# Performance work log

Hardware: AMD Instinct MI355X
Metric: run time of the kernel (lower is better)

Reference implementation:

```python
import jax, jax.numpy as jnp
import numpy as np
from jax import lax

HID = 128      # GNN hidden dim (node_label_embedding_size)
EMB = 64       # char-CNN output (graph_node_label_representation_size)
N_LAYERS = 6
N_ETYPES = 12
CHAR_EMB = 16
KW = 5         # conv kernel width
LEAKY = 0.2


def _gru(x, h, k, rk, b):
    # keras-style GRU cell: gates z, r, candidate hh; new h = z*h + (1-z)*hh
    H = h.shape[-1]
    g = x @ k + b                       # [N, 3H]
    z = jax.nn.sigmoid(g[:, :H] + h @ rk[:, :H])
    r = jax.nn.sigmoid(g[:, H:2 * H] + h @ rk[:, H:2 * H])
    hh = jnp.tanh(g[:, 2 * H:] + (r * h) @ rk[:, 2 * H:])
    return z * h + (1.0 - z) * hh


def setup_inputs() -> dict:
    key = jax.random.key(0)
    ks = jax.random.split(key, 32)
    N, U, L, E, G = 100000, 20000, 16, 100000, 64
    inp = {}
    inp["graphs_in_batch"] = G
    inp["node_labels_unique"] = jax.random.randint(ks[0], (U, L), 0, 256, dtype=jnp.int32)
    inp["node_labels_index"] = jax.random.randint(ks[1], (N,), 0, U, dtype=jnp.int32)
    inp["node_to_graph"] = jnp.sort(jax.random.randint(ks[2], (N,), 0, G, dtype=jnp.int32))
    inp["regression_labels"] = jax.random.normal(ks[3], (G,), dtype=jnp.float32)
    for t in range(N_ETYPES):
        inp[f"adj_{t}"] = jax.random.randint(ks[4 + t], (E, 2), 0, N, dtype=jnp.int32)
    # learned params
    inp["char_embed"] = jax.random.normal(ks[16], (256, CHAR_EMB), dtype=jnp.float32) * 0.1
    inp["conv_w"] = jax.random.normal(ks[17], (KW, CHAR_EMB, EMB), dtype=jnp.float32) / np.sqrt(KW * CHAR_EMB)
    inp["conv_b"] = jnp.zeros((EMB,), dtype=jnp.float32)
    inp["W_msg"] = jax.random.normal(ks[18], (N_LAYERS, N_ETYPES, HID, HID), dtype=jnp.float32) / np.sqrt(HID)
    inp["gru_k"] = jax.random.normal(ks[19], (N_LAYERS, HID, 3 * HID), dtype=jnp.float32) / np.sqrt(HID)
    inp["gru_rk"] = jax.random.normal(ks[20], (N_LAYERS, HID, 3 * HID), dtype=jnp.float32) / np.sqrt(HID)
    inp["gru_b"] = jnp.zeros((N_LAYERS, 3 * HID), dtype=jnp.float32)
    inp["score_w"] = jax.random.normal(ks[21], (HID, 1), dtype=jnp.float32) / np.sqrt(HID)
    inp["score_b"] = jnp.zeros((1,), dtype=jnp.float32)
    inp["mlp_w1"] = jax.random.normal(ks[22], (HID, 128), dtype=jnp.float32) / np.sqrt(HID)
    inp["mlp_b1"] = jnp.zeros((128,), dtype=jnp.float32)
    inp["mlp_w2"] = jax.random.normal(ks[23], (128, 32), dtype=jnp.float32) / np.sqrt(128)
    inp["mlp_b2"] = jnp.zeros((32,), dtype=jnp.float32)
    inp["mlp_w3"] = jax.random.normal(ks[24], (32, 8), dtype=jnp.float32) / np.sqrt(32)
    inp["mlp_b3"] = jnp.zeros((8,), dtype=jnp.float32)
    inp["mlp_w4"] = jax.random.normal(ks[25], (8, 1), dtype=jnp.float32) / np.sqrt(8)
    inp["mlp_b4"] = jnp.zeros((1,), dtype=jnp.float32)
    return inp


def reference(graphs_in_batch, node_labels_unique, node_labels_index, node_to_graph,
              regression_labels, adj_0, adj_1, adj_2, adj_3, adj_4, adj_5, adj_6,
              adj_7, adj_8, adj_9, adj_10, adj_11, char_embed, conv_w, conv_b,
              W_msg, gru_k, gru_rk, gru_b, score_w, score_b,
              mlp_w1, mlp_b1, mlp_w2, mlp_b2, mlp_w3, mlp_b3, mlp_w4, mlp_b4):
    adj = jnp.stack([adj_0, adj_1, adj_2, adj_3, adj_4, adj_5, adj_6,
                     adj_7, adj_8, adj_9, adj_10, adj_11])  # [T, E, 2]
    # --- char-CNN node label embedding ---
    chars = char_embed[node_labels_unique]                  # [U, L, CE]
    conv = lax.conv_general_dilated(chars, conv_w, (1,), 'SAME',
                                    dimension_numbers=('NWC', 'WIO', 'NWC'))
    label_rep = jnp.max(jax.nn.relu(conv + conv_b), axis=1)  # [U, EMB]
    feats = label_rep[node_labels_index]                     # [N, EMB]
    N = feats.shape[0]
    # pad initial features up to hidden_dim
    h = jnp.pad(feats, ((0, 0), (0, HID - EMB)))             # [N, HID]
    src = adj[:, :, 0]                                       # [T, E]
    tgt = adj[:, :, 1].reshape(-1)                           # [T*E]
    # --- 6-layer GGNN message passing ---
    for layer in range(N_LAYERS):
        h_src = h[src]                                       # [T, E, HID]
        msgs = jnp.einsum('teh,thd->ted', h_src, W_msg[layer])
        agg = jax.ops.segment_sum(msgs.reshape(-1, HID), tgt, num_segments=N)
        h = _gru(agg, h, gru_k[layer], gru_rk[layer], gru_b[layer])
    # --- weighted-sum graph readout (sigmoid weights, leaky_relu MLP) ---
    scores = jax.nn.sigmoid(h @ score_w + score_b)           # [N, 1]
    v = jax.nn.leaky_relu(h @ mlp_w1 + mlp_b1, LEAKY)
    v = jax.nn.leaky_relu(v @ mlp_w2 + mlp_b2, LEAKY)
    v = jax.nn.leaky_relu(v @ mlp_w3 + mlp_b3, LEAKY)
    v = v @ mlp_w4 + mlp_b4                                  # [N, 1]
    graph_rep = jax.ops.segment_sum(scores * v, node_to_graph,
                                    num_segments=graphs_in_batch)  # [G, 1]
    return graph_rep
```

## Files before the change

kernel.cpp:

```cpp
#include <hip/hip_runtime.h>
#include <hip/hip_bf16.h>

#define LEAKY_SLOPE 0.2f

typedef short short8 __attribute__((ext_vector_type(8)));
typedef float f32x4 __attribute__((ext_vector_type(4)));

static inline int cdiv(int a, int b) { return (a + b - 1) / b; }

__device__ __forceinline__ float bf2f(unsigned short s) {
    return __uint_as_float(((unsigned int)s) << 16);
}
__device__ __forceinline__ unsigned short f2bf(float x) {
    unsigned int u = __float_as_uint(x);
    return (unsigned short)((u + 0x7FFFu + ((u >> 16) & 1u)) >> 16);
}
__device__ __forceinline__ unsigned short bf_hi(float x, float& rem) {
    unsigned int u = __float_as_uint(x);
    unsigned int hi = (u + 0x7FFFu + ((u >> 16) & 1u)) & 0xFFFF0000u;
    rem = x - __uint_as_float(hi);
    return (unsigned short)(hi >> 16);
}

struct EdgeArgs {
    const int* adj[12];
    int E[12];
    int colOff[12];
};
struct ColPtrs { const int* c[12]; };
struct MutColPtrs { int* c[12]; };

__global__ __launch_bounds__(64) void label_kernel(
    const int* __restrict__ labels, const float* __restrict__ char_embed,
    const float* __restrict__ conv_w, const float* __restrict__ conv_b,
    float* __restrict__ lr, int U)
{
    __shared__ float ch[20][16];
    __shared__ int lab[16];
    const int u = blockIdx.x, t = threadIdx.x;
    {
        const int r = t >> 4, i = t & 15;
        const int padrow[4] = {0, 1, 18, 19};
        ch[padrow[r]][i] = 0.f;
    }
    if (t < 16) lab[t] = labels[(size_t)u * 16 + t];
    float cwr[5][16];
    #pragma unroll
    for (int k = 0; k < 5; ++k)
        #pragma unroll
        for (int i = 0; i < 16; ++i)
            cwr[k][i] = conv_w[(k * 16 + i) * 64 + t];
    __syncthreads();
    for (int j = t; j < 256; j += 64)
        ch[2 + (j >> 4)][j & 15] = char_embed[(size_t)lab[j >> 4] * 16 + (j & 15)];
    __syncthreads();
    float aw[16];
    const float b = conv_b[t];
    #pragma unroll
    for (int w = 0; w < 16; ++w) aw[w] = b;
    #pragma unroll
    for (int x = 0; x < 20; ++x)
        #pragma unroll
        for (int i = 0; i < 16; ++i) {
            const float chv = ch[x][i];
            #pragma unroll
            for (int k = 0; k < 5; ++k) {
                const int w = x - k;
                if (w >= 0 && w < 16) aw[w] += chv * cwr[k][i];
            }
        }
    float m = 0.f;
    #pragma unroll
    for (int w = 0; w < 16; ++w) m = fmaxf(m, aw[w]);
    lr[(size_t)u * 64 + t] = m;
}

__global__ void init_hP(const int* __restrict__ idx, const float* __restrict__ lr,
                        unsigned short* __restrict__ hP, int N, int NP)
{
    const int i = blockIdx.x * blockDim.x + threadIdx.x;
    if (i >= NP * 16) return;
    const int n = i >> 4, kg = i & 15;
    short8 hi, lo;
    #pragma unroll
    for (int j = 0; j < 8; ++j) { hi[j] = 0; lo[j] = 0; }
    if (n < N && kg < 8) {
        const int id = idx[n];
        #pragma unroll
        for (int j = 0; j < 8; ++j) {
            const float v = lr[(size_t)id * 64 + kg * 8 + j];
            float r; hi[j] = (short)bf_hi(v, r); lo[j] = (short)f2bf(r);
        }
    }
    *(short8*)(hP + (size_t)n * 256 + kg * 16) = hi;
    *(short8*)(hP + (size_t)n * 256 + kg * 16 + 8) = lo;
}

__global__ void hist_kernel(EdgeArgs ea, int* __restrict__ deg, int N)
{
    const int t = blockIdx.y;
    const int e = blockIdx.x * blockDim.x + threadIdx.x;
    if (e >= ea.E[t]) return;
    atomicAdd(&deg[(size_t)t * N + ea.adj[t][2 * e + 1]], 1);
}

__global__ __launch_bounds__(256) void scan_a(const int* __restrict__ deg,
                                              int* __restrict__ partial, int N, int nchunk)
{
    const int t = blockIdx.y, b = blockIdx.x;
    const int base = b * 2048;
    int s = 0;
    for (int i = threadIdx.x; i < 2048; i += 256) {
        const int g = base + i;
        if (g < N) s += deg[(size_t)t * N + g];
    }
    __shared__ int sm[256];
    sm[threadIdx.x] = s; __syncthreads();
    for (int off = 128; off > 0; off >>= 1) {
        if (threadIdx.x < off) sm[threadIdx.x] += sm[threadIdx.x + off];
        __syncthreads();
    }
    if (threadIdx.x == 0) partial[t * nchunk + b] = sm[0];
}

__global__ void scan_b(int* __restrict__ partial, int nchunk)
{
    const int t = threadIdx.x;
    if (t >= 12) return;
    int off = 0;
    for (int i = 0; i < nchunk; ++i) {
        const int s = partial[t * nchunk + i];
        partial[t * nchunk + i] = off;
        off += s;
    }
}

__global__ __launch_bounds__(256) void scan_c(const int* __restrict__ deg,
                                              const int* __restrict__ partial,
                                              int* __restrict__ rowptr, int N, int nchunk)
{
    const int t = blockIdx.y, b = blockIdx.x;
    int* rp = rowptr + (size_t)t * (N + 1);
    const int base = b * 2048;
    int v[8]; int s = 0;
    #pragma unroll
    for (int j = 0; j < 8; ++j) {
        const int g = base + threadIdx.x * 8 + j;
        v[j] = (g < N) ? deg[(size_t)t * N + g] : 0;
        s += v[j];
    }
    __shared__ int ts[256];
    ts[threadIdx.x] = s; __syncthreads();
    for (int off = 1; off < 256; off <<= 1) {
        const int val = (threadIdx.x >= off) ? ts[threadIdx.x - off] : 0;
        __syncthreads();
        ts[threadIdx.x] += val;
        __syncthreads();
    }
    int run = partial[t * nchunk + b] + (threadIdx.x ? ts[threadIdx.x - 1] : 0);
    #pragma unroll
    for (int j = 0; j < 8; ++j) {
        const int g = base + threadIdx.x * 8 + j;
        run += v[j];
        if (g < N) rp[g + 1] = run;
    }
    if (b == 0 && threadIdx.x == 0) rp[0] = 0;
}

__global__ void fill_kernel(EdgeArgs ea, const int* __restrict__ rowptr,
                            int* __restrict__ cursor, int* __restrict__ col, int N)
{
    const int t = blockIdx.y;
    const int e = blockIdx.x * blockDim.x + threadIdx.x;
    if (e >= ea.E[t]) return;
    const int s  = ea.adj[t][2 * e];
    const int tg = ea.adj[t][2 * e + 1];
    const int pos = rowptr[(size_t)t * (N + 1) + tg] + atomicAdd(&cursor[(size_t)t * N + tg], 1);
    col[ea.colOff[t] + pos] = s;
}

__global__ __launch_bounds__(256) void sort_cols_kernel(
    const int* __restrict__ rowptr, MutColPtrs mc, int N)
{
    const int t = blockIdx.y;
    const int r = blockIdx.x * blockDim.x + threadIdx.x;
    if (r >= N) return;
    int* c = mc.c[t];
    const int s = rowptr[(size_t)t * (N + 1) + r];
    const int e = rowptr[(size_t)t * (N + 1) + r + 1];
    for (int i = s + 1; i < e; ++i) {
        const int key = c[i];
        int j = i - 1;
        while (j >= s && c[j] > key) { c[j + 1] = c[j]; --j; }
        c[j + 1] = key;
    }
}

struct WSrc { const float* wmsg; const float* gk; const float* grk; const float* w1; };

__global__ void split_w_kernel(WSrc s, unsigned short* __restrict__ wb, int nmat)
{
    const int gidx = blockIdx.x * 256 + threadIdx.x;
    const int m = gidx >> 14, e = gidx & 16383;
    if (m >= nmat) return;
    const int kg = e >> 10, rem = e & 1023, c = rem >> 3, j = rem & 7;
    const int k = kg * 8 + j;
    float x;
    if (m < 72) x = s.wmsg[(size_t)m * 16384 + (size_t)k * 128 + c];
    else if (m < 108) {
        const int g = m - 72, layer = g / 6, r2 = g % 6;
        const float* base = (r2 < 3) ? s.gk : s.grk;
        const int slice = r2 % 3;
        x = base[(size_t)layer * 49152 + (size_t)k * 384 + slice * 128 + c];
    } else x = s.w1[(size_t)k * 128 + c];
    float r; const unsigned short hi = bf_hi(x, r);
    wb[(size_t)m * 32768 + e] = hi;
    wb[(size_t)m * 32768 + 16384 + e] = f2bf(r);
}

__global__ __launch_bounds__(256) void agg_kernel(
    const unsigned short* __restrict__ hP,
    const int* __restrict__ rowptr, ColPtrs cps,
    const unsigned short* __restrict__ wbL,
    float* __restrict__ agg, int N)
{
    __shared__ unsigned short Sf[32768];
    const int tid = threadIdx.x, p = blockIdx.x;
    const int R0 = p * 128;
    const int wave = tid >> 6, lane = tid & 63;
    const int wr = wave >> 1, wc = wave & 1, lrow = lane & 15, lkg = lane >> 4;
    const int rhalf = tid >> 2;
    const int j4 = tid & 3;
    f32x4 acc[4][4] = {};

    for (int t = 0; t < 12; ++t) {
        const int* __restrict__ rp_t = rowptr + (size_t)t * (N + 1);
        const int* __restrict__ cl = cps.c[t];
        #pragma unroll
        for (int half = 0; half < 2; ++half) {
            const int row = half * 64 + rhalf;
            const int R = R0 + row;
            float ga[32];
            #pragma unroll
            for (int j = 0; j < 32; ++j) ga[j] = 0.f;
            if (R < N) {
                const int e1 = rp_t[R + 1];
                for (int e = rp_t[R]; e < e1; ++e) {
                    const unsigned short* hp = hP + (size_t)cl[e] * 256 + j4 * 64;
                    #pragma unroll
                    for (int c = 0; c < 4; ++c) {
                        const short8 hh = *(const short8*)(hp + c * 16);
                        const short8 hl = *(const short8*)(hp + c * 16 + 8);
                        #pragma unroll
                        for (int q = 0; q < 8; ++q)
                            ga[c * 8 + q] += bf2f((unsigned short)hh[q])
                                           + bf2f((unsigned short)hl[q]);
                    }
                }
            }
            #pragma unroll
            for (int c = 0; c < 4; ++c) {
                const int kg = j4 * 4 + c;
                short8 hi, lo;
                #pragma unroll
                for (int q = 0; q < 8; ++q) {
                    float rem;
                    hi[q] = (short)bf_hi(ga[c * 8 + q], rem);
                    lo[q] = (short)f2bf(rem);
                }
                const int u = ((kg << 10) + row * 8) ^ (kg << 3);
                *(short8*)(Sf + u) = hi;
                *(short8*)(Sf + u + 16384) = lo;
            }
        }
        __syncthreads();
        {
            const unsigned short* __restrict__ B = wbL + (size_t)t * 32768;
            #pragma unroll
            for (int q = 0; q < 4; ++q) {
                const int kg = q * 4 + lkg;
                short8 ah[4], al[4];
                #pragma unroll
                for (int m = 0; m < 4; ++m) {
                    const int u = ((kg << 10) + (wr * 64 + m * 16 + lrow) * 8) ^ (kg << 3);
                    ah[m] = *(const short8*)(Sf + u);
                    al[m] = *(const short8*)(Sf + u + 16384);
                }
                #pragma unroll
                for (int n = 0; n < 4; ++n) {
                    const int ub = kg * 1024 + (wc * 64 + n * 16 + lrow) * 8;
                    const short8 bh = *(const short8*)(B + ub);
                    const short8 bl = *(const short8*)(B + ub + 16384);
                    #pragma unroll
                    for (int m = 0; m < 4; ++m) {
                        acc[m][n] = __builtin_amdgcn_mfma_f32_16x16x32_bf16(ah[m], bh, acc[m][n], 0, 0, 0);
                        acc[m][n] = __builtin_amdgcn_mfma_f32_16x16x32_bf16(ah[m], bl, acc[m][n], 0, 0, 0);
                        acc[m][n] = __builtin_amdgcn_mfma_f32_16x16x32_bf16(al[m], bh, acc[m][n], 0, 0, 0);
                    }
                }
            }
        }
        __syncthreads();
    }

    #pragma unroll
    for (int m = 0; m < 4; ++m)
        #pragma unroll
        for (int n = 0; n < 4; ++n) {
            const int col = wc * 64 + n * 16 + lrow;
            #pragma unroll
            for (int i = 0; i < 4; ++i) {
                const size_t Rg = (size_t)p * 128 + wr * 64 + m * 16 + lkg * 4 + i;
                agg[Rg * 128 + col] = acc[m][n][i];
            }
        }
}

__global__ __launch_bounds__(256) void zr2_kernel(
    const float* __restrict__ aggf, const unsigned short* __restrict__ hP,
    const unsigned short* __restrict__ k0, const unsigned short* __restrict__ k1,
    const unsigned short* __restrict__ rk0, const unsigned short* __restrict__ rk1,
    const float* __restrict__ bias,
    float* __restrict__ Zf, unsigned short* __restrict__ rhP)
{
    __shared__ unsigned short lds[2][8192];
    const int tid = threadIdx.x, p = blockIdx.x;
    const int wave = tid >> 6, lane = tid & 63;
    const int wr = wave >> 1, wc = wave & 1, lrow = lane & 15, lkg = lane >> 4;
    f32x4 acc[2][4][4] = {};
    float fv[16];
    short8 ph[2], pl[2];

    auto ldq = [&](int s) {
        const int q = s & 3;
        #pragma unroll
        for (int j = 0; j < 2; ++j) {
            const int cid = j * 256 + tid, kgl = cid >> 7, row = cid & 127;
            if (s < 4) {
                const float* a = aggf + ((size_t)p * 128 + row) * 128 + q * 32 + kgl * 8;
                const float4 v0 = *(const float4*)(a);
                const float4 v1 = *(const float4*)(a + 4);
                fv[j*8+0]=v0.x; fv[j*8+1]=v0.y; fv[j*8+2]=v0.z; fv[j*8+3]=v0.w;
                fv[j*8+4]=v1.x; fv[j*8+5]=v1.y; fv[j*8+6]=v1.z; fv[j*8+7]=v1.w;
            } else {
                const unsigned short* hp = hP + ((size_t)p * 128 + row) * 256 + (q * 4 + kgl) * 16;
                ph[j] = *(const short8*)(hp);
                pl[j] = *(const short8*)(hp + 8);
            }
        }
    };
    auto stq = [&](int buf, int s) {
        unsigned short* L = lds[buf];
        #pragma unroll
        for (int j = 0; j < 2; ++j) {
            const int cid = j * 256 + tid, kgl = cid >> 7, row = cid & 127;
            const int u = (kgl * 1024 + row * 8) ^ (kgl << 3);
            short8 hi, lo;
            if (s < 4) {
                #pragma unroll
                for (int q8 = 0; q8 < 8; ++q8) {
                    float rem; hi[q8] = (short)bf_hi(fv[j*8+q8], rem); lo[q8] = (short)f2bf(rem);
                }
            } else { hi = ph[j]; lo = pl[j]; }
            *(short8*)(L + u) = hi;
            *(short8*)(L + u + 4096) = lo;
        }
    };
    auto mfma_q = [&](int buf, int s) {
        const unsigned short* L = lds[buf];
        const int q = s & 3;
        short8 ah[4], al[4];
        #pragma unroll
        for (int m = 0; m < 4; ++m) {
            const int u = ((lkg << 10) + (wr * 64 + m * 16 + lrow) * 8) ^ (lkg << 3);
            ah[m] = *(const short8*)(L + u);
            al[m] = *(const short8*)(L + u + 4096);
        }
        const unsigned short* Bt[2] = { (s < 4) ? k0 : rk0, (s < 4) ? k1 : rk1 };
        #pragma unroll
        for (int t = 0; t < 2; ++t) {
            const unsigned short* __restrict__ B = Bt[t];
            #pragma unroll
            for (int n = 0; n < 4; ++n) {
                const int ub = (q * 4 + lkg) * 1024 + (wc * 64 + n * 16 + lrow) * 8;
                const short8 bh = *(const short8*)(B + ub);
                const short8 bl = *(const short8*)(B + ub + 16384);
                #pragma unroll
                for (int m = 0; m < 4; ++m) {
                    acc[t][m][n] = __builtin_amdgcn_mfma_f32_16x16x32_bf16(ah[m], bh, acc[t][m][n], 0, 0, 0);
                    acc[t][m][n] = __builtin_amdgcn_mfma_f32_16x16x32_bf16(ah[m], bl, acc[t][m][n], 0, 0, 0);
                    acc[t][m][n] = __builtin_amdgcn_mfma_f32_16x16x32_bf16(al[m], bh, acc[t][m][n], 0, 0, 0);
                }
            }
        }
    };

    ldq(0); stq(0, 0); ldq(1);
    __syncthreads();
    #pragma unroll
    for (int s = 0; s < 8; ++s) {
        mfma_q(s & 1, s);
        if (s < 7) {
            stq((s + 1) & 1, s + 1);
            if (s < 6) ldq(s + 2);
            __syncthreads();
        }
    }

    #pragma unroll
    for (int m = 0; m < 4; ++m)
        #pragma unroll
        for (int n = 0; n < 4; ++n) {
            const int col = wc * 64 + n * 16 + lrow;
            #pragma unroll
            for (int i = 0; i < 4; ++i) {
                const int rl = wr * 64 + m * 16 + lkg * 4 + i;
                const size_t R = (size_t)p * 128 + rl;
                const float z = 1.f / (1.f + __expf(-(acc[0][m][n][i] + bias[col])));
                Zf[R * 128 + col] = z;
                const float r = 1.f / (1.f + __expf(-(acc[1][m][n][i] + bias[128 + col])));
                const size_t hu = R * 256 + (size_t)(col >> 3) * 16 + (col & 7);
                const float h = bf2f(hP[hu]) + bf2f(hP[hu + 8]);
                float rem; const unsigned short hh = bf_hi(r * h, rem);
                rhP[hu] = hh;
                rhP[hu + 8] = f2bf(rem);
            }
        }
}

__global__ __launch_bounds__(256) void g2_kernel(
    const float* __restrict__ aggf, const unsigned short* __restrict__ rhP,
    const unsigned short* __restrict__ k2, const unsigned short* __restrict__ rk2,
    const float* __restrict__ bias, const float* __restrict__ Zf,
    unsigned short* __restrict__ hP)
{
    __shared__ unsigned short lds[2][8192];
    const int tid = threadIdx.x, p = blockIdx.x;
    const int wave = tid >> 6, lane = tid & 63;
    const int wr = wave >> 1, wc = wave & 1, lrow = lane & 15, lkg = lane >> 4;
    f32x4 acc[4][4] = {};
    float fv[16];
    short8 ph[2], pl[2];

    auto ldq = [&](int s) {
        const int q = s & 3;
        #pragma unroll
        for (int j = 0; j < 2; ++j) {
            const int cid = j * 256 + tid, kgl = cid >> 7, row = cid & 127;
            if (s < 4) {
                const float* a = aggf + ((size_t)p * 128 + row) * 128 + q * 32 + kgl * 8;
                const float4 v0 = *(const float4*)(a);
                const float4 v1 = *(const float4*)(a + 4);
                fv[j*8+0]=v0.x; fv[j*8+1]=v0.y; fv[j*8+2]=v0.z; fv[j*8+3]=v0.w;
                fv[j*8+4]=v1.x; fv[j*8+5]=v1.y; fv[j*8+6]=v1.z; fv[j*8+7]=v1.w;
            } else {
                const unsigned short* hp = rhP + ((size_t)p * 128 + row) * 256 + (q * 4 + kgl) * 16;
                ph[j] = *(const short8*)(hp);
                pl[j] = *(const short8*)(hp + 8);
            }
        }
    };
    auto stq = [&](int buf, int s) {
        unsigned short* L = lds[buf];
        #pragma unroll
        for (int j = 0; j < 2; ++j) {
            const int cid = j * 256 + tid, kgl = cid >> 7, row = cid & 127;
            const int u = (kgl * 1024 + row * 8) ^ (kgl << 3);
            short8 hi, lo;
            if (s < 4) {
                #pragma unroll
                for (int q8 = 0; q8 < 8; ++q8) {
                    float rem; hi[q8] = (short)bf_hi(fv[j*8+q8], rem); lo[q8] = (short)f2bf(rem);
                }
            } else { hi = ph[j]; lo = pl[j]; }
            *(short8*)(L + u) = hi;
            *(short8*)(L + u + 4096) = lo;
        }
    };
    auto mfma_q = [&](int buf, int s) {
        const unsigned short* L = lds[buf];
        const int q = s & 3;
        short8 ah[4], al[4];
        #pragma unroll
        for (int m = 0; m < 4; ++m) {
            const int u = ((lkg << 10) + (wr * 64 + m * 16 + lrow) * 8) ^ (lkg << 3);
            ah[m] = *(const short8*)(L + u);
            al[m] = *(const short8*)(L + u + 4096);
        }
        const unsigned short* __restrict__ B = (s < 4) ? k2 : rk2;
        #pragma unroll
        for (int n = 0; n < 4; ++n) {
            const int ub = (q * 4 + lkg) * 1024 + (wc * 64 + n * 16 + lrow) * 8;
            const short8 bh = *(const short8*)(B + ub);
            const short8 bl = *(const short8*)(B + ub + 16384);
            #pragma unroll
            for (int m = 0; m < 4; ++m) {
                acc[m][n] = __builtin_amdgcn_mfma_f32_16x16x32_bf16(ah[m], bh, acc[m][n], 0, 0, 0);
                acc[m][n] = __builtin_amdgcn_mfma_f32_16x16x32_bf16(ah[m], bl, acc[m][n], 0, 0, 0);
                acc[m][n] = __builtin_amdgcn_mfma_f32_16x16x32_bf16(al[m], bh, acc[m][n], 0, 0, 0);
            }
        }
    };

    ldq(0); stq(0, 0); ldq(1);
    __syncthreads();
    #pragma unroll
    for (int s = 0; s < 8; ++s) {
        mfma_q(s & 1, s);
        if (s < 7) {
            stq((s + 1) & 1, s + 1);
            if (s < 6) ldq(s + 2);
            __syncthreads();
        }
    }

    #pragma unroll
    for (int m = 0; m < 4; ++m)
        #pragma unroll
        for (int n = 0; n < 4; ++n) {
            const int col = wc * 64 + n * 16 + lrow;
            #pragma unroll
            for (int i = 0; i < 4; ++i) {
                const int rl = wr * 64 + m * 16 + lkg * 4 + i;
                const size_t R = (size_t)p * 128 + rl;
                const float g = acc[m][n][i] + bias[col];
                const size_t hu = R * 256 + (size_t)(col >> 3) * 16 + (col & 7);
                const float h = bf2f(hP[hu]) + bf2f(hP[hu + 8]);
                const float z = Zf[R * 128 + col];
                const float hn = z * h + (1.f - z) * tanhf(g);
                float rem; const unsigned short hh = bf_hi(hn, rem);
                hP[hu] = hh;
                hP[hu + 8] = f2bf(rem);
            }
        }
}

__global__ __launch_bounds__(256) void v1_kernel(
    const unsigned short* __restrict__ hP, const unsigned short* __restrict__ w1b,
    const float* __restrict__ bias, float* __restrict__ outF)
{
    __shared__ unsigned short lds[2][8192];
    const int tid = threadIdx.x, p = blockIdx.x;
    const int wave = tid >> 6, lane = tid & 63;
    const int wr = wave >> 1, wc = wave & 1, lrow = lane & 15, lkg = lane >> 4;
    f32x4 acc[4][4] = {};
    short8 ph[2], pl[2];

    auto ldq = [&](int s) {
        #pragma unroll
        for (int j = 0; j < 2; ++j) {
            const int cid = j * 256 + tid, kgl = cid >> 7, row = cid & 127;
            const unsigned short* hp = hP + ((size_t)p * 128 + row) * 256 + (s * 4 + kgl) * 16;
            ph[j] = *(const short8*)(hp);
            pl[j] = *(const short8*)(hp + 8);
        }
    };
    auto stq = [&](int buf) {
        unsigned short* L = lds[buf];
        #pragma unroll
        for (int j = 0; j < 2; ++j) {
            const int cid = j * 256 + tid, kgl = cid >> 7, row = cid & 127;
            const int u = (kgl * 1024 + row * 8) ^ (kgl << 3);
            *(short8*)(L + u) = ph[j];
            *(short8*)(L + u + 4096) = pl[j];
        }
    };
    auto mfma_q = [&](int buf, int s) {
        const unsigned short* L = lds[buf];
        short8 ah[4], al[4];
        #pragma unroll
        for (int m = 0; m < 4; ++m) {
            const int u = ((lkg << 10) + (wr * 64 + m * 16 + lrow) * 8) ^ (lkg << 3);
            ah[m] = *(const short8*)(L + u);
            al[m] = *(const short8*)(L + u + 4096);
        }
        #pragma unroll
        for (int n = 0; n < 4; ++n) {
            const int ub = (s * 4 + lkg) * 1024 + (wc * 64 + n * 16 + lrow) * 8;
            const short8 bh = *(const short8*)(w1b + ub);
            const short8 bl = *(const short8*)(w1b + ub + 16384);
            #pragma unroll
            for (int m = 0; m < 4; ++m) {
                acc[m][n] = __builtin_amdgcn_mfma_f32_16x16x32_bf16(ah[m], bh, acc[m][n], 0, 0, 0);
                acc[m][n] = __builtin_amdgcn_mfma_f32_16x16x32_bf16(ah[m], bl, acc[m][n], 0, 0, 0);
                acc[m][n] = __builtin_amdgcn_mfma_f32_16x16x32_bf16(al[m], bh, acc[m][n], 0, 0, 0);
            }
        }
    };

    ldq(0); stq(0); ldq(1);
    __syncthreads();
    #pragma unroll
    for (int s = 0; s < 4; ++s) {
        mfma_q(s & 1, s);
        if (s < 3) {
            stq((s + 1) & 1);
            if (s < 2) ldq(s + 2);
            __syncthreads();
        }
    }

    #pragma unroll
    for (int m = 0; m < 4; ++m)
        #pragma unroll
        for (int n = 0; n < 4; ++n) {
            const int col = wc * 64 + n * 16 + lrow;
            #pragma unroll
            for (int i = 0; i < 4; ++i) {
                const size_t R = (size_t)p * 128 + wr * 64 + m * 16 + lkg * 4 + i;
                float v = acc[m][n][i] + bias[col];
                v = v > 0.f ? v : LEAKY_SLOPE * v;
                outF[R * 128 + col] = v;
            }
        }
}

__global__ __launch_bounds__(256) void final_kernel(
    const unsigned short* __restrict__ hP, const float* __restrict__ V1,
    const int* __restrict__ n2g,
    const float* __restrict__ w2, const float* __restrict__ b2,
    const float* __restrict__ w3, const float* __restrict__ b3,
    const float* __restrict__ w4, const float* __restrict__ b4,
    const float* __restrict__ score_w, const float* __restrict__ score_b,
    float* __restrict__ out, int N)
{
    const int n = blockIdx.x * blockDim.x + threadIdx.x;
    const int nc = n < N ? n : N - 1;
    const int g = n2g[nc];

    float sp = score_b[0];
    #pragma unroll 4
    for (int kg = 0; kg < 16; ++kg) {
        const size_t hu = (size_t)nc * 256 + kg * 16;
        const short8 hh = *(const short8*)(hP + hu);
        const short8 hl = *(const short8*)(hP + hu + 8);
        #pragma unroll
        for (int j = 0; j < 8; ++j)
            sp += (bf2f((unsigned short)hh[j]) + bf2f((unsigned short)hl[j])) * score_w[kg * 8 + j];
    }

    float V2[32];
    #pragma unroll
    for (int j = 0; j < 32; ++j) V2[j] = b2[j];
    #pragma unroll 2
    for (int k = 0; k < 128; k += 4) {
        const float4 v1 = *reinterpret_cast<const float4*>(V1 + (size_t)nc * 128 + k);
        const float vv[4] = {v1.x, v1.y, v1.z, v1.w};
        #pragma unroll
        for (int kk = 0; kk < 4; ++kk)
            #pragma unroll
            for (int j = 0; j < 32; ++j)
                V2[j] += vv[kk] * w2[(k + kk) * 32 + j];
    }
    #pragma unroll
    for (int j = 0; j < 32; ++j) { const float x = V2[j]; V2[j] = x > 0.f ? x : LEAKY_SLOPE * x; }

    float V3[8];
    #pragma unroll
    for (int j = 0; j < 8; ++j) V3[j] = b3[j];
    #pragma unroll
    for (int k = 0; k < 32; ++k)
        #pragma unroll
        for (int j = 0; j < 8; ++j) V3[j] += V2[k] * w3[k * 8 + j];
    #pragma unroll
    for (int j = 0; j < 8; ++j) { const float x = V3[j]; V3[j] = x > 0.f ? x : LEAKY_SLOPE * x; }

    float o4 = b4[0];
    #pragma unroll
    for (int j = 0; j < 8; ++j) o4 += V3[j] * w4[j];

    const float sc = 1.f / (1.f + __expf(-sp));
    float val = (n < N) ? sc * o4 : 0.f;

    const int g0 = __shfl(g, 0, 64);
    if (__all(g == g0)) {
        #pragma unroll
        for (int d = 32; d > 0; d >>= 1) val += __shfl_xor(val, d, 64);
        if ((threadIdx.x & 63) == 0) unsafeAtomicAdd(out + g0, val);
    } else {
        if (n < N) unsafeAtomicAdd(out + g, val);
    }
}

extern "C" void kernel_launch(void* const* d_in, const int* in_sizes, int n_in,
                              void* d_out, int out_size, void* d_ws, size_t ws_size,
                              hipStream_t stream)
{
    (void)n_in;
    const int* labels   = (const int*)d_in[1];
    const int* nidx     = (const int*)d_in[2];
    const int* n2g      = (const int*)d_in[3];
    EdgeArgs ea;
    int Emax = 0, Etot = 0;
    for (int t = 0; t < 12; ++t) {
        ea.adj[t] = (const int*)d_in[5 + t];
        ea.E[t] = in_sizes[5 + t] / 2;
        ea.colOff[t] = Etot;
        Etot += ea.E[t];
        if (ea.E[t] > Emax) Emax = ea.E[t];
    }
    const float* char_embed = (const float*)d_in[17];
    const float* conv_w     = (const float*)d_in[18];
    const float* conv_b     = (const float*)d_in[19];
    const float* W_msg      = (const float*)d_in[20];
    const float* gru_k      = (const float*)d_in[21];
    const float* gru_rk     = (const float*)d_in[22];
    const float* gru_b      = (const float*)d_in[23];
    const float* score_w    = (const float*)d_in[24];
    const float* score_b    = (const float*)d_in[25];
    const float* w1 = (const float*)d_in[26];
    const float* b1 = (const float*)d_in[27];
    const float* w2 = (const float*)d_in[28];
    const float* b2 = (const float*)d_in[29];
    const float* w3 = (const float*)d_in[30];
    const float* b3 = (const float*)d_in[31];
    const float* w4 = (const float*)d_in[32];
    const float* b4 = (const float*)d_in[33];

    const int N = in_sizes[2];
    const int U = in_sizes[1] / 16;
    const int G = out_size;
    float* out = (float*)d_out;

    const int NPB = cdiv(N, 128);
    const int NP  = NPB * 128;
    const int NCHUNK = cdiv(N, 2048);
    const int NMAT = 109;

    float* ws = (float*)d_ws;
    size_t o = 0;
    float* lr   = ws + o; o += (size_t)U * 64;
    float* hPf  = ws + o; o += (size_t)NP * 128;
    float* aggf = ws + o; o += (size_t)NP * 128;
    float* Zf   = ws + o; o += (size_t)NP * 128;
    float* rhPf = ws + o; o += (size_t)NP * 128;
    float* wbf  = ws + o; o += (size_t)NMAT * 16384;
    int* rowptr = (int*)(ws + o);
    int* colarr = rowptr + (size_t)12 * (N + 1);
    const size_t total_bytes = o * sizeof(float)
        + ((size_t)12 * (N + 1) + (size_t)Etot) * sizeof(int);
    if (total_bytes > ws_size) return;

    unsigned short* hP  = (unsigned short*)hPf;
    unsigned short* rhP = (unsigned short*)rhPf;
    unsigned short* wb  = (unsigned short*)wbf;

    int* deg     = (int*)Zf;
    int* cursor  = deg + (size_t)12 * N;
    int* partial = cursor + (size_t)12 * N;

    hipMemsetAsync(d_out, 0, (size_t)G * sizeof(float), stream);
    hipMemsetAsync(deg, 0, ((size_t)24 * N + 12 * NCHUNK) * sizeof(int), stream);

    MutColPtrs mcp;
    ColPtrs cps;
    for (int t = 0; t < 12; ++t) {
        mcp.c[t] = colarr + ea.colOff[t];
        cps.c[t] = colarr + ea.colOff[t];
    }

    {
        const dim3 ge(cdiv(Emax, 256), 12);
        const dim3 gs(NCHUNK, 12);
        const dim3 gn(cdiv(N, 256), 12);
        hist_kernel<<<ge, 256, 0, stream>>>(ea, deg, N);
        scan_a<<<gs, 256, 0, stream>>>(deg, partial, N, NCHUNK);
        scan_b<<<1, 64, 0, stream>>>(partial, NCHUNK);
        scan_c<<<gs, 256, 0, stream>>>(deg, partial, rowptr, N, NCHUNK);
        fill_kernel<<<ge, 256, 0, stream>>>(ea, rowptr, cursor, colarr, N);
        sort_cols_kernel<<<gn, 256, 0, stream>>>(rowptr, mcp, N);
    }

    WSrc wsrc{W_msg, gru_k, gru_rk, w1};
    split_w_kernel<<<cdiv(NMAT * 16384, 256), 256, 0, stream>>>(wsrc, wb, NMAT);
    label_kernel<<<U, 64, 0, stream>>>(labels, char_embed, conv_w, conv_b, lr, U);
    init_hP<<<cdiv(NP * 16, 256), 256, 0, stream>>>(nidx, lr, hP, N, NP);

    auto wbm = [&](int m) { return wb + (size_t)m * 32768; };

    for (int layer = 0; layer < 6; ++layer) {
        const float* bl = gru_b + (size_t)layer * 384;
        const int mk = 72 + layer * 6;
        agg_kernel<<<NPB, 256, 0, stream>>>(hP, rowptr, cps,
                                            wbm(layer * 12), aggf, N);
        zr2_kernel<<<NPB, 256, 0, stream>>>(aggf, hP, wbm(mk + 0), wbm(mk + 1),
                                            wbm(mk + 3), wbm(mk + 4), bl, Zf, rhP);
        g2_kernel<<<NPB, 256, 0, stream>>>(aggf, rhP, wbm(mk + 2), wbm(mk + 5),
                                           bl + 256, Zf, hP);
    }
    v1_kernel<<<NPB, 256, 0, stream>>>(hP, wbm(108), b1, Zf);
    final_kernel<<<cdiv(N, 256), 256, 0, stream>>>(hP, Zf, n2g, w2, b2, w3, b3, w4, b4,
                                                   score_w, score_b, out, N);
}
```

Before: 3.765 ms.

## Fuse GRU gate and candidate kernels into one per-tile kernel

Merges the z/r gate kernel and the candidate/update kernel into a single kernel. The x·k2 product is accumulated alongside z and r, r*h is staged through LDS in split bf16, and the final rk2 GEMM and state update run in the same block. This removes the Zf and rhP global round-trips, one launch per layer, and the reloading of aggf. In exchange it holds three accumulator sets in registers and uses a larger LDS allocation, which may lower occupancy. hP is read and written in place, which is safe only because each block touches just its own rows.

```diff
diff --git a/kernel.cpp b/kernel.cpp
--- a/kernel.cpp
+++ b/kernel.cpp
@@ -316,18 +316,20 @@
         }
 }
 
-__global__ __launch_bounds__(256) void zr2_kernel(
-    const float* __restrict__ aggf, const unsigned short* __restrict__ hP,
+__global__ __launch_bounds__(256) void zrg_kernel(
+    const float* __restrict__ aggf, const unsigned short* __restrict__ hPc,
     const unsigned short* __restrict__ k0, const unsigned short* __restrict__ k1,
+    const unsigned short* __restrict__ k2,
     const unsigned short* __restrict__ rk0, const unsigned short* __restrict__ rk1,
+    const unsigned short* __restrict__ rk2,
     const float* __restrict__ bias,
-    float* __restrict__ Zf, unsigned short* __restrict__ rhP)
-{
-    __shared__ unsigned short lds[2][8192];
+    unsigned short* __restrict__ hP)
+{
+    __shared__ unsigned short lds[32768];
     const int tid = threadIdx.x, p = blockIdx.x;
     const int wave = tid >> 6, lane = tid & 63;
     const int wr = wave >> 1, wc = wave & 1, lrow = lane & 15, lkg = lane >> 4;
-    f32x4 acc[2][4][4] = {};
+    f32x4 accZ[4][4] = {}, accR[4][4] = {}, accG[4][4] = {};
     float fv[16];
     short8 ph[2], pl[2];
 
@@ -343,14 +345,14 @@
                 fv[j*8+0]=v0.x; fv[j*8+1]=v0.y; fv[j*8+2]=v0.z; fv[j*8+3]=v0.w;
                 fv[j*8+4]=v1.x; fv[j*8+5]=v1.y; fv[j*8+6]=v1.z; fv[j*8+7]=v1.w;
             } else {
-                const unsigned short* hp = hP + ((size_t)p * 128 + row) * 256 + (q * 4 + kgl) * 16;
+                const unsigned short* hp = hPc + ((size_t)p * 128 + row) * 256 + (q * 4 + kgl) * 16;
                 ph[j] = *(const short8*)(hp);
                 pl[j] = *(const short8*)(hp + 8);
             }
         }
     };
     auto stq = [&](int buf, int s) {
-        unsigned short* L = lds[buf];
+        unsigned short* L = lds + buf * 8192;
         #pragma unroll
         for (int j = 0; j < 2; ++j) {
             const int cid = j * 256 + tid, kgl = cid >> 7, row = cid & 127;
@@ -367,7 +369,7 @@
         }
     };
     auto mfma_q = [&](int buf, int s) {
-        const unsigned short* L = lds[buf];
+        const unsigned short* L = lds + buf * 8192;
         const int q = s & 3;
         short8 ah[4], al[4];
         #pragma unroll
@@ -376,20 +378,39 @@
             ah[m] = *(const short8*)(L + u);
             al[m] = *(const short8*)(L + u + 4096);
         }
-        const unsigned short* Bt[2] = { (s < 4) ? k0 : rk0, (s < 4) ? k1 : rk1 };
-        #pragma unroll
-        for (int t = 0; t < 2; ++t) {
-            const unsigned short* __restrict__ B = Bt[t];
-            #pragma unroll
-            for (int n = 0; n < 4; ++n) {
-                const int ub = (q * 4 + lkg) * 1024 + (wc * 64 + n * 16 + lrow) * 8;
-                const short8 bh = *(const short8*)(B + ub);
-                const short8 bl = *(const short8*)(B + ub + 16384);
+        const unsigned short* B0 = (s < 4) ? k0 : rk0;
+        const unsigned short* B1 = (s < 4) ? k1 : rk1;
+        #pragma unroll
+        for (int n = 0; n < 4; ++n) {
+            const int ub = (q * 4 + lkg) * 1024 + (wc * 64 + n * 16 + lrow) * 8;
+            {
+                const short8 bh = *(const short8*)(B0 + ub);
+                const short8 bl = *(const short8*)(B0 + ub + 16384);
                 #pragma unroll
                 for (int m = 0; m < 4; ++m) {
-                    acc[t][m][n] = __builtin_amdgcn_mfma_f32_16x16x32_bf16(ah[m], bh, acc[t][m][n], 0, 0, 0);
-                    acc[t][m][n] = __builtin_amdgcn_mfma_f32_16x16x32_bf16(ah[m], bl, acc[t][m][n], 0, 0, 0);
-                    acc[t][m][n] = __builtin_amdgcn_mfma_f32_16x16x32_bf16(al[m], bh, acc[t][m][n], 0, 0, 0);
+                    accZ[m][n] = __builtin_amdgcn_mfma_f32_16x16x32_bf16(ah[m], bh, accZ[m][n], 0, 0, 0);
+                    accZ[m][n] = __builtin_amdgcn_mfma_f32_16x16x32_bf16(ah[m], bl, accZ[m][n], 0, 0, 0);
+                    accZ[m][n] = __builtin_amdgcn_mfma_f32_16x16x32_bf16(al[m], bh, accZ[m][n], 0, 0, 0);
+                }
+            }
+            {
+                const short8 bh = *(const short8*)(B1 + ub);
+                const short8 bl = *(const short8*)(B1 + ub + 16384);
+                #pragma unroll
+                for (int m = 0; m < 4; ++m) {
+                    accR[m][n] = __builtin_amdgcn_mfma_f32_16x16x32_bf16(ah[m], bh, accR[m][n], 0, 0, 0);
+                    accR[m][n] = __builtin_amdgcn_mfma_f32_16x16x32_bf16(ah[m], bl, accR[m][n], 0, 0, 0);
+                    accR[m][n] = __builtin_amdgcn_mfma_f32_16x16x32_bf16(al[m], bh, accR[m][n], 0, 0, 0);
+                }
+            }
+            if (s < 4) {
+                const short8 bh = *(const short8*)(k2 + ub);
+                const short8 bl = *(const short8*)(k2 + ub + 16384);
+                #pragma unroll
+                for (int m = 0; m < 4; ++m) {
+                    accG[m][n] = __builtin_amdgcn_mfma_f32_16x16x32_bf16(ah[m], bh, accG[m][n], 0, 0, 0);
+                    accG[m][n] = __builtin_amdgcn_mfma_f32_16x16x32_bf16(ah[m], bl, accG[m][n], 0, 0, 0);
+                    accG[m][n] = __builtin_amdgcn_mfma_f32_16x16x32_bf16(al[m], bh, accG[m][n], 0, 0, 0);
                 }
             }
         }
@@ -407,110 +428,53 @@
         }
     }
 
+    __syncthreads();
     #pragma unroll
     for (int m = 0; m < 4; ++m)
         #pragma unroll
         for (int n = 0; n < 4; ++n) {
             const int col = wc * 64 + n * 16 + lrow;
+            const int kg = col >> 3;
             #pragma unroll
             for (int i = 0; i < 4; ++i) {
                 const int rl = wr * 64 + m * 16 + lkg * 4 + i;
                 const size_t R = (size_t)p * 128 + rl;
-                const float z = 1.f / (1.f + __expf(-(acc[0][m][n][i] + bias[col])));
-                Zf[R * 128 + col] = z;
-                const float r = 1.f / (1.f + __expf(-(acc[1][m][n][i] + bias[128 + col])));
-                const size_t hu = R * 256 + (size_t)(col >> 3) * 16 + (col & 7);
-                const float h = bf2f(hP[hu]) + bf2f(hP[hu + 8]);
-                float rem; const unsigned short hh = bf_hi(r * h, rem);
-                rhP[hu] = hh;
-                rhP[hu + 8] = f2bf(rem);
-            }
-        }
-}
-
-__global__ __launch_bounds__(256) void g2_kernel(
-    const float* __restrict__ aggf, const unsigned short* __restrict__ rhP,
-    const unsigned short* __restrict__ k2, const unsigned short* __restrict__ rk2,
-    const float* __restrict__ bias, const float* __restrict__ Zf,
-    unsigned short* __restrict__ hP)
-{
-    __shared__ unsigned short lds[2][8192];
-    const int tid = threadIdx.x, p = blockIdx.x;
-    const int wave = tid >> 6, lane = tid & 63;
-    const int wr = wave >> 1, wc = wave & 1, lrow = lane & 15, lkg = lane >> 4;
-    f32x4 acc[4][4] = {};
-    float fv[16];
-    short8 ph[2], pl[2];
-
-    auto ldq = [&](int s) {
-        const int q = s & 3;
-        #pragma unroll
-        for (int j = 0; j < 2; ++j) {
-            const int cid = j * 256 + tid, kgl = cid >> 7, row = cid & 127;
-            if (s < 4) {
-                const float* a = aggf + ((size_t)p * 128 + row) * 128 + q * 32 + kgl * 8;
-                const float4 v0 = *(const float4*)(a);
-                const float4 v1 = *(const float4*)(a + 4);
-                fv[j*8+0]=v0.x; fv[j*8+1]=v0.y; fv[j*8+2]=v0.z; fv[j*8+3]=v0.w;
-                fv[j*8+4]=v1.x; fv[j*8+5]=v1.y; fv[j*8+6]=v1.z; fv[j*8+7]=v1.w;
-            } else {
-                const unsigned short* hp = rhP + ((size_t)p * 128 + row) * 256 + (q * 4 + kgl) * 16;
-                ph[j] = *(const short8*)(hp);
-                pl[j] = *(const short8*)(hp + 8);
-            }
-        }
-    };
-    auto stq = [&](int buf, int s) {
-        unsigned short* L = lds[buf];
-        #pragma unroll
-        for (int j = 0; j < 2; ++j) {
-            const int cid = j * 256 + tid, kgl = cid >> 7, row = cid & 127;
-            const int u = (kgl * 1024 + row * 8) ^ (kgl << 3);
-            short8 hi, lo;
-            if (s < 4) {
-                #pragma unroll
-                for (int q8 = 0; q8 < 8; ++q8) {
-                    float rem; hi[q8] = (short)bf_hi(fv[j*8+q8], rem); lo[q8] = (short)f2bf(rem);
-                }
-            } else { hi = ph[j]; lo = pl[j]; }
-            *(short8*)(L + u) = hi;
-            *(short8*)(L + u + 4096) = lo;
-        }
-    };
-    auto mfma_q = [&](int buf, int s) {
-        const unsigned short* L = lds[buf];
-        const int q = s & 3;
+                const float z = 1.f / (1.f + __expf(-(accZ[m][n][i] + bias[col])));
+                const float r = 1.f / (1.f + __expf(-(accR[m][n][i] + bias[128 + col])));
+                const size_t hu = R * 256 + (size_t)kg * 16 + (col & 7);
+                const float h = bf2f(hPc[hu]) + bf2f(hPc[hu + 8]);
+                accZ[m][n][i] = z;
+                accR[m][n][i] = h;
+                const float rh = r * h;
+                float rem;
+                const int u = ((kg << 10) + rl * 8 + (col & 7)) ^ (kg << 3);
+                lds[u] = bf_hi(rh, rem);
+                lds[u + 16384] = f2bf(rem);
+            }
+        }
+    __syncthreads();
+
+    #pragma unroll
+    for (int q = 0; q < 4; ++q) {
+        const int kg = q * 4 + lkg;
         short8 ah[4], al[4];
         #pragma unroll
         for (int m = 0; m < 4; ++m) {
-            const int u = ((lkg << 10) + (wr * 64 + m * 16 + lrow) * 8) ^ (lkg << 3);
-            ah[m] = *(const short8*)(L + u);
-            al[m] = *(const short8*)(L + u + 4096);
-        }
-        const unsigned short* __restrict__ B = (s < 4) ? k2 : rk2;
+            const int u = ((kg << 10) + (wr * 64 + m * 16 + lrow) * 8) ^ (kg << 3);
+            ah[m] = *(const short8*)(lds + u);
+            al[m] = *(const short8*)(lds + u + 16384);
+        }
         #pragma unroll
         for (int n = 0; n < 4; ++n) {
-            const int ub = (q * 4 + lkg) * 1024 + (wc * 64 + n * 16 + lrow) * 8;
-            const short8 bh = *(const short8*)(B + ub);
-            const short8 bl = *(const short8*)(B + ub + 16384);
+            const int ub = kg * 1024 + (wc * 64 + n * 16 + lrow) * 8;
+            const short8 bh = *(const short8*)(rk2 + ub);
+            const short8 bl = *(const short8*)(rk2 + ub + 16384);
             #pragma unroll
             for (int m = 0; m < 4; ++m) {
-                acc[m][n] = __builtin_amdgcn_mfma_f32_16x16x32_bf16(ah[m], bh, acc[m][n], 0, 0, 0);
-                acc[m][n] = __builtin_amdgcn_mfma_f32_16x16x32_bf16(ah[m], bl, acc[m][n], 0, 0, 0);
-                acc[m][n] = __builtin_amdgcn_mfma_f32_16x16x32_bf16(al[m], bh, acc[m][n], 0, 0, 0);
-            }
-        }
-    };
-
-    ldq(0); stq(0, 0); ldq(1);
-    __syncthreads();
-    #pragma unroll
-    for (int s = 0; s < 8; ++s) {
-        mfma_q(s & 1, s);
-        if (s < 7) {
-            stq((s + 1) & 1, s + 1);
-            if (s < 6) ldq(s + 2);
-            __syncthreads();
+                accG[m][n] = __builtin_amdgcn_mfma_f32_16x16x32_bf16(ah[m], bh, accG[m][n], 0, 0, 0);
+                accG[m][n] = __builtin_amdgcn_mfma_f32_16x16x32_bf16(ah[m], bl, accG[m][n], 0, 0, 0);
+                accG[m][n] = __builtin_amdgcn_mfma_f32_16x16x32_bf16(al[m], bh, accG[m][n], 0, 0, 0);
+            }
         }
     }
 
@@ -523,11 +487,11 @@
             for (int i = 0; i < 4; ++i) {
                 const int rl = wr * 64 + m * 16 + lkg * 4 + i;
                 const size_t R = (size_t)p * 128 + rl;
-                const float g = acc[m][n][i] + bias[col];
+                const float g = accG[m][n][i] + bias[256 + col];
+                const float z = accZ[m][n][i];
+                const float h = accR[m][n][i];
+                const float hn = z * h + (1.f - z) * tanhf(g);
                 const size_t hu = R * 256 + (size_t)(col >> 3) * 16 + (col & 7);
-                const float h = bf2f(hP[hu]) + bf2f(hP[hu + 8]);
-                const float z = Zf[R * 128 + col];
-                const float hn = z * h + (1.f - z) * tanhf(g);
                 float rem; const unsigned short hh = bf_hi(hn, rem);
                 hP[hu] = hh;
                 hP[hu + 8] = f2bf(rem);
@@ -732,8 +696,6 @@
     float* lr   = ws + o; o += (size_t)U * 64;
     float* hPf  = ws + o; o += (size_t)NP * 128;
     float* aggf = ws + o; o += (size_t)NP * 128;
-    float* Zf   = ws + o; o += (size_t)NP * 128;
-    float* rhPf = ws + o; o += (size_t)NP * 128;
     float* wbf  = ws + o; o += (size_t)NMAT * 16384;
     int* rowptr = (int*)(ws + o);
     int* colarr = rowptr + (size_t)12 * (N + 1);
@@ -741,11 +703,10 @@
         + ((size_t)12 * (N + 1) + (size_t)Etot) * sizeof(int);
     if (total_bytes > ws_size) return;
 
-    unsigned short* hP  = (unsigned short*)hPf;
-    unsigned short* rhP = (unsigned short*)rhPf;
-    unsigned short* wb  = (unsigned short*)wbf;
-
-    int* deg     = (int*)Zf;
+    unsigned short* hP = (unsigned short*)hPf;
+    unsigned short* wb = (unsigned short*)wbf;
+
+    int* deg     = (int*)aggf;
     int* cursor  = deg + (size_t)12 * N;
     int* partial = cursor + (size_t)12 * N;
 
@@ -783,12 +744,12 @@
         const int mk = 72 + layer * 6;
         agg_kernel<<<NPB, 256, 0, stream>>>(hP, rowptr, cps,
                                             wbm(layer * 12), aggf, N);
-        zr2_kernel<<<NPB, 256, 0, stream>>>(aggf, hP, wbm(mk + 0), wbm(mk + 1),
-                                            wbm(mk + 3), wbm(mk + 4), bl, Zf, rhP);
-        g2_kernel<<<NPB, 256, 0, stream>>>(aggf, rhP, wbm(mk + 2), wbm(mk + 5),
-                                           bl + 256, Zf, hP);
-    }
-    v1_kernel<<<NPB, 256, 0, stream>>>(hP, wbm(108), b1, Zf);
-    final_kernel<<<cdiv(N, 256), 256, 0, stream>>>(hP, Zf, n2g, w2, b2, w3, b3, w4, b4,
+        zrg_kernel<<<NPB, 256, 0, stream>>>(aggf, hP,
+                                            wbm(mk + 0), wbm(mk + 1), wbm(mk + 2),
+                                            wbm(mk + 3), wbm(mk + 4), wbm(mk + 5),
+                                            bl, hP);
+    }
+    v1_kernel<<<NPB, 256, 0, stream>>>(hP, wbm(108), b1, aggf);
+    final_kernel<<<cdiv(N, 256), 256, 0, stream>>>(hP, aggf, n2g, w2, b2, w3, b3, w4, b4,
                                                    score_w, score_b, out, N);
 }
```

New measurement: 3.648 ms (median of 2 runs). 1.03x faster.
